# Kernel tuning notes

Hardware: AMD Instinct MI355X
Metric: run time of the kernel (lower is better)

Reference implementation:

```python
import jax, jax.numpy as jnp
import numpy as np

V, E, H, L, B, T = 50000, 512, 512, 32, 64, 512


def _lstm_dir(xg, w_hh, reverse):
    # xg: [B,T,4H] precomputed input-to-gate projections (+ biases)
    b, t, g4 = xg.shape
    h_dim = g4 // 4
    def step(carry, xt):
        h, c = carry
        g = xt + h @ w_hh.T  # [B,4H], PyTorch gate order i,f,g,o
        i, f, gg, o = jnp.split(g, 4, axis=-1)
        c = jax.nn.sigmoid(f) * c + jax.nn.sigmoid(i) * jnp.tanh(gg)
        h = jax.nn.sigmoid(o) * jnp.tanh(c)
        return (h, c), h
    init = (jnp.zeros((b, h_dim), xg.dtype), jnp.zeros((b, h_dim), xg.dtype))
    _, hs = jax.lax.scan(step, init, jnp.swapaxes(xg, 0, 1), reverse=reverse)
    return jnp.swapaxes(hs, 0, 1)  # [B,T,H]


def _bilstm(x, w_ih0, w_ih1, w_hh, b_ih, b_hh):
    w_ihs = (w_ih0, w_ih1)
    for l in range(2):
        outs = []
        for d in range(2):  # 0=forward, 1=backward
            xg = jnp.einsum('bti,gi->btg', x, w_ihs[l][d]) + b_ih[l, d] + b_hh[l, d]
            outs.append(_lstm_dir(xg, w_hh[l, d], reverse=(d == 1)))
        x = jnp.concatenate(outs, axis=-1)  # [B,T,2H]
    return x


def _crf_nll(emissions, tags, start, end, trans):
    # pytorch-crf: returns sum log-likelihood; module returns its negation.
    emit = jnp.take_along_axis(emissions, tags[..., None], axis=-1)[..., 0]  # [B,T]
    num = (start[tags[:, 0]] + emit.sum(1)
           + trans[tags[:, :-1], tags[:, 1:]].sum(1) + end[tags[:, -1]])
    alpha0 = start + emissions[:, 0]  # [B,L]
    def step(alpha, e_t):
        s = alpha[:, :, None] + trans[None] + e_t[:, None, :]  # [B,L,L]
        return jax.nn.logsumexp(s, axis=1), None
    alpha, _ = jax.lax.scan(step, alpha0, jnp.swapaxes(emissions[:, 1:], 0, 1))
    denom = jax.nn.logsumexp(alpha + end, axis=-1)  # [B]
    return -(num - denom).sum()


def setup_inputs() -> dict:
    key = jax.random.key(0)
    ks = jax.random.split(key, 13)
    s = 0.05
    emb = jax.random.normal(ks[0], (V, E), jnp.float32) * s
    emb = emb.at[0].set(0.0)  # padding_idx=0
    return {
        'datas': jax.random.randint(ks[1], (B, T), 0, V, jnp.int32),
        'labels': jax.random.randint(ks[2], (B, T), 0, L, jnp.int32),
        'emb': emb,
        'w_ih0': jax.random.normal(ks[3], (2, 4 * H, E), jnp.float32) * s,
        'w_ih1': jax.random.normal(ks[4], (2, 4 * H, 2 * H), jnp.float32) * s,
        'w_hh': jax.random.normal(ks[5], (2, 2, 4 * H, H), jnp.float32) * s,
        'b_ih': jax.random.normal(ks[6], (2, 2, 4 * H), jnp.float32) * s,
        'b_hh': jax.random.normal(ks[7], (2, 2, 4 * H), jnp.float32) * s,
        'w_out': jax.random.normal(ks[8], (2 * H, L), jnp.float32) * s,
        'b_out': jax.random.normal(ks[9], (L,), jnp.float32) * s,
        'crf_start': jax.random.normal(ks[10], (L,), jnp.float32) * s,
        'crf_end': jax.random.normal(ks[11], (L,), jnp.float32) * s,
        'crf_trans': jax.random.normal(ks[12], (L, L), jnp.float32) * s,
    }


def reference(datas, labels, emb, w_ih0, w_ih1, w_hh, b_ih, b_hh, w_out, b_out,
              crf_start, crf_end, crf_trans):
    x = emb[datas]  # [B,T,E]
    h = _bilstm(x, w_ih0, w_ih1, w_hh, b_ih, b_hh)  # [B,T,2H]; dropout=0 (eval)
    emissions = h @ w_out + b_out  # [B,T,L]
    return _crf_nll(emissions, labels, crf_start, crf_end, crf_trans)
```

## Files before the change

kernel.cpp:

```cpp
#include <hip/hip_runtime.h>

typedef unsigned short ushort_t;
typedef unsigned long long u64_t;
typedef __attribute__((ext_vector_type(8))) short short8;
typedef __attribute__((ext_vector_type(4))) float floatx4;


__device__ __forceinline__ float bf2f(ushort_t u) {
  unsigned x = ((unsigned)u) << 16;
  return __builtin_bit_cast(float, x);
}
__device__ __forceinline__ ushort_t f2bf(float f) {
  unsigned x = __builtin_bit_cast(unsigned, f);
  x += 0x7FFFu + ((x >> 16) & 1u);
  return (ushort_t)(x >> 16);
}
__device__ __forceinline__ float sigf(float x) { return 1.0f / (1.0f + __expf(-x)); }
__device__ __forceinline__ float tanhf_(float x) { return 1.0f - 2.0f / (__expf(2.0f * x) + 1.0f); }

static const size_t OFF_A    = 0;
static const size_t OFF_OUT0 = 67108864;
static const size_t OFF_XG   = 134217728;
static const size_t OFF_WIH0 = 167772160;
static const size_t OFF_WIH1 = 171966464;
static const size_t OFF_BIAS = 180355072;
static const size_t OFF_WOUT = 180387840;
static const size_t OFF_HC   = 180453376;
static const size_t OFF_CST  = 181501952;
static const size_t OFF_BAR  = 182026240;
static const size_t OFF_NUM  = 182059008;
static const size_t OFF_PERB = 182059264;
static const size_t OFF_END  = 182059520;

__global__ void prep_kernel(const float* __restrict__ w_ih0, const float* __restrict__ w_ih1,
                            const float* __restrict__ b_ih, const float* __restrict__ b_hh,
                            const float* __restrict__ w_out,
                            ushort_t* __restrict__ wih0_bf, ushort_t* __restrict__ wih1_bf,
                            float* __restrict__ bias, ushort_t* __restrict__ wout_bf) {
  int idx = blockIdx.x * 256 + threadIdx.x;
  int stride = gridDim.x * 256;
  for (int i = idx; i < 2097152; i += stride) wih0_bf[i] = f2bf(w_ih0[i]);
  for (int i = idx; i < 4194304; i += stride) wih1_bf[i] = f2bf(w_ih1[i]);
  for (int i = idx; i < 8192; i += stride) bias[i] = b_ih[i] + b_hh[i];
  for (int i = idx; i < 32768; i += stride) {
    int j = i & 7, Ls = (i >> 3) & 63, kb = (i >> 9) & 31, nt = i >> 14;
    int n = nt * 16 + (Ls & 15);
    int k = kb * 32 + ((Ls >> 4) & 3) * 8 + j;
    wout_bf[i] = f2bf(w_out[k * 32 + n]);
  }
}

__global__ void embed_kernel(const int* __restrict__ datas, const float* __restrict__ emb,
                             ushort_t* __restrict__ x_bf) {
  int idx = blockIdx.x * 256 + threadIdx.x;
  int row = idx >> 6, sub = idx & 63;
  int tok = datas[row];
  const float4* ep = (const float4*)(emb + (size_t)tok * 512 + sub * 8);
  float4 f0 = ep[0], f1 = ep[1];
  short8 v;
  v[0] = (short)f2bf(f0.x); v[1] = (short)f2bf(f0.y);
  v[2] = (short)f2bf(f0.z); v[3] = (short)f2bf(f0.w);
  v[4] = (short)f2bf(f1.x); v[5] = (short)f2bf(f1.y);
  v[6] = (short)f2bf(f1.z); v[7] = (short)f2bf(f1.w);
  *(short8*)(x_bf + (size_t)row * 512 + sub * 8) = v;
}

__device__ __forceinline__ void gemm_body(ushort_t* alds, ushort_t* blds, int gid, int tid,
                                          const ushort_t* __restrict__ A, int K,
                                          const ushort_t* __restrict__ W,
                                          const float* __restrict__ biasL,
                                          ushort_t* __restrict__ xg0,
                                          ushort_t* __restrict__ xg1,
                                          int t00, int t01) {
  int dir = gid >> 9, r = gid & 511;
  int mt = r & 31, ntt = r >> 5;
  int t0 = dir ? t01 : t00;
  const ushort_t* Bm = W + (size_t)dir * 2048 * K;
  const float* bptr = biasL + dir * 2048;
  ushort_t* xg = dir ? xg1 : xg0;
  int bm0 = mt * 128, bn0 = ntt * 128;
  int L = tid & 63, w = tid >> 6;
  int wm = w & 1, wn = w >> 1;
  floatx4 acc[4][4] = {};
  for (int k0 = 0; k0 < K; k0 += 32) {
    __syncthreads();
    #pragma unroll
    for (int rep = 0; rep < 2; rep++) {
      int slot = rep * 256 + tid;
      int t8 = slot >> 6, Ls = slot & 63;
      int col = k0 + (Ls >> 4) * 8;
      int mp = bm0 + t8 * 16 + (Ls & 15);
      int Arow = (mp >> 6) * 512 + t0 + (mp & 63);
      *(short8*)&alds[slot * 8] = *(const short8*)&A[(size_t)Arow * K + col];
      int rowb = bn0 + t8 * 16 + (Ls & 15);
      *(short8*)&blds[slot * 8] = *(const short8*)&Bm[(size_t)rowb * K + col];
    }
    __syncthreads();
    short8 af[4];
    #pragma unroll
    for (int a = 0; a < 4; a++) af[a] = *(const short8*)&alds[((wm * 4 + a) * 64 + L) * 8];
    #pragma unroll
    for (int bq = 0; bq < 4; bq++) {
      short8 bfr = *(const short8*)&blds[((wn * 4 + bq) * 64 + L) * 8];
      #pragma unroll
      for (int a = 0; a < 4; a++)
        acc[a][bq] = __builtin_amdgcn_mfma_f32_16x16x32_bf16(af[a], bfr, acc[a][bq], 0, 0, 0);
    }
  }
  int lm = L >> 4, ln = L & 15;
  #pragma unroll
  for (int bq = 0; bq < 4; bq++) {
    int n = bn0 + (wn * 4 + bq) * 16 + ln;
    float bv = bptr[n];
    #pragma unroll
    for (int a = 0; a < 4; a++) {
      #pragma unroll
      for (int rr = 0; rr < 4; rr++) {
        int m = bm0 + (wm * 4 + a) * 16 + lm * 4 + rr;
        int b = m >> 6, ts = m & 63;
        xg[((size_t)(ts * 64 + b)) * 2048 + n] = f2bf(acc[a][bq][rr] + bv);
      }
    }
  }
}

__global__ __launch_bounds__(256) void gemm_chunk(const ushort_t* __restrict__ A, int K,
                                                  const ushort_t* __restrict__ W,
                                                  const float* __restrict__ biasL,
                                                  ushort_t* __restrict__ xg0c,
                                                  ushort_t* __restrict__ xg1c,
                                                  int t00, int t01) {
  __shared__ alignas(16) ushort_t alds[512 * 8];
  __shared__ alignas(16) ushort_t blds[512 * 8];
  gemm_body(alds, blds, blockIdx.x, threadIdx.x, A, K, W, biasL, xg0c, xg1c, t00, t01);
}

__device__ __forceinline__ void lstm_body(ushort_t* wlds, int bid, int tid,
                                          const ushort_t* __restrict__ xg0c,
                                          const ushort_t* __restrict__ xg1c,
                                          const float* __restrict__ whh_f,
                                          ushort_t* __restrict__ hcL,
                                          float* __restrict__ cstL,
                                          ushort_t* __restrict__ outL,
                                          int* __restrict__ barF, int c) {
  int d = bid >> 5, g = bid & 31, j0 = g * 16;
  int L = tid & 63, w = tid >> 6;
  const float* wptr = whh_f + (size_t)d * 2048 * 512;
  #pragma unroll
  for (int it = 0; it < 16; it++) {
    int slot = it * 256 + tid;
    int q = slot >> 10, kb = (slot >> 6) & 15, Ls = slot & 63;
    int gcol = q * 512 + j0 + (Ls & 15);
    int k = kb * 32 + (Ls >> 4) * 8;
    const float* src = wptr + (size_t)gcol * 512 + k;
    float4 f0 = *(const float4*)src;
    float4 f1 = *(const float4*)(src + 4);
    short8 v;
    v[0] = (short)f2bf(f0.x); v[1] = (short)f2bf(f0.y);
    v[2] = (short)f2bf(f0.z); v[3] = (short)f2bf(f0.w);
    v[4] = (short)f2bf(f1.x); v[5] = (short)f2bf(f1.y);
    v[6] = (short)f2bf(f1.z); v[7] = (short)f2bf(f1.w);
    *(short8*)&wlds[slot * 8] = v;
  }
  __syncthreads();
  const ushort_t* xgd = d ? xg1c : xg0c;
  ushort_t* hcd = hcL + (size_t)d * 2 * 32768;
  int* flg = barF + d * 2048;
  int* myflag = flg + (g * 4 + w) * 16;
  const int* pollp = flg + ((L & 31) * 4 + w) * 16;
  bool pact = (L < 32);
  int q8 = L >> 4, jj = L & 15;
  int mbase = w * 16 + q8 * 4;
  int wslot = ((w * 16 + (g >> 1)) * 64 + q8 * 4 + 16 * ((g & 1) * 2 + (jj >> 3))) * 8 + (jj & 7);
  int rbase = (w * 16 * 64 + L) * 8;
  float cv[4];
  #pragma unroll
  for (int rr = 0; rr < 4; rr++) cv[rr] = cstL[(size_t)d * 32768 + (mbase + rr) * 512 + j0 + jj];

  auto ldxg = [&](int sl2, ushort_t dst[4][4]) {
    int ts2 = d ? (63 - sl2) : sl2;
    #pragma unroll
    for (int rr = 0; rr < 4; rr++) {
      const ushort_t* xrow = xgd + ((size_t)(ts2 * 64 + mbase + rr)) * 2048 + j0 + jj;
      #pragma unroll
      for (int q = 0; q < 4; q++) dst[q][rr] = xrow[q * 512];
    }
  };

  ushort_t xgu[4][4];
  ldxg(0, xgu);

  for (int sl = 0; sl < 64; sl++) {
    int s = c * 64 + sl;
    int t = d ? (511 - s) : s;
    const u64_t* h64 = (const u64_t*)(hcd + (size_t)(s & 1) * 32768);
    unsigned* h32w = (unsigned*)(hcd + (size_t)((s + 1) & 1) * 32768);
    int b64 = rbase >> 2;
    u64_t hv[32];
    #pragma unroll
    for (int kb = 0; kb < 16; kb++) {
      hv[2 * kb]     = __hip_atomic_load(h64 + b64 + kb * 128,     __ATOMIC_RELAXED, __HIP_MEMORY_SCOPE_AGENT);
      hv[2 * kb + 1] = __hip_atomic_load(h64 + b64 + kb * 128 + 1, __ATOMIC_RELAXED, __HIP_MEMORY_SCOPE_AGENT);
    }
    floatx4 acc[4] = {};
    #pragma unroll
    for (int kb = 0; kb < 16; kb++) {
      union { u64_t u[2]; short8 v; } pk;
      pk.u[0] = hv[2 * kb];
      pk.u[1] = hv[2 * kb + 1];
      short8 a = pk.v;
      #pragma unroll
      for (int q = 0; q < 4; q++) {
        short8 bfr = *(const short8*)&wlds[((q * 16 + kb) * 64 + L) * 8];
        acc[q] = __builtin_amdgcn_mfma_f32_16x16x32_bf16(a, bfr, acc[q], 0, 0, 0);
      }
    }
    ushort_t hbv[4];
    #pragma unroll
    for (int rr = 0; rr < 4; rr++) {
      float ii = acc[0][rr] + bf2f(xgu[0][rr]);
      float ff = acc[1][rr] + bf2f(xgu[1][rr]);
      float gg = acc[2][rr] + bf2f(xgu[2][rr]);
      float oo = acc[3][rr] + bf2f(xgu[3][rr]);
      float cc = sigf(ff) * cv[rr] + sigf(ii) * tanhf_(gg);
      cv[rr] = cc;
      hbv[rr] = f2bf(sigf(oo) * tanhf_(cc));
    }
    bool evn = (jj & 1) == 0;
    unsigned pk4[4];
    #pragma unroll
    for (int rr = 0; rr < 4; rr++) {
      unsigned mine = (unsigned)hbv[rr];
      unsigned nb = (unsigned)__shfl_xor((int)mine, 1, 64);
      pk4[rr] = mine | (nb << 16);
      if (evn)
        __hip_atomic_store(h32w + ((wslot + rr * 8) >> 1), pk4[rr],
                           __ATOMIC_RELAXED, __HIP_MEMORY_SCOPE_AGENT);
    }
    if (sl != 63) {
      asm volatile("s_waitcnt vmcnt(0)" ::: "memory");
      if (L == 0)
        __hip_atomic_store(myflag, s + 1, __ATOMIC_RELAXED, __HIP_MEMORY_SCOPE_AGENT);
      if (evn) {
        #pragma unroll
        for (int rr = 0; rr < 4; rr++) {
          int m = mbase + rr;
          *(unsigned*)&outL[((size_t)m * 512 + t) * 1024 + (d << 9) + j0 + jj] = pk4[rr];
        }
      }
      ldxg(sl + 1, xgu);
      int target = s + 1, guard = 0;
      while (guard < (1 << 17)) {
        int f = pact ? __hip_atomic_load(pollp, __ATOMIC_RELAXED, __HIP_MEMORY_SCOPE_AGENT)
                     : target;
        if (__ballot(f >= target) == ~0ULL) break;
        guard++;
      }
    } else {
      if (evn) {
        #pragma unroll
        for (int rr = 0; rr < 4; rr++) {
          int m = mbase + rr;
          *(unsigned*)&outL[((size_t)m * 512 + t) * 1024 + (d << 9) + j0 + jj] = pk4[rr];
        }
      }
    }
  }
  #pragma unroll
  for (int rr = 0; rr < 4; rr++) cstL[(size_t)d * 32768 + (mbase + rr) * 512 + j0 + jj] = cv[rr];
}

__global__ __launch_bounds__(256) void lstm_chunk(const ushort_t* __restrict__ xg0c,
                                                  const ushort_t* __restrict__ xg1c,
                                                  const float* __restrict__ whh_f,
                                                  ushort_t* __restrict__ hcL,
                                                  float* __restrict__ cstL,
                                                  ushort_t* __restrict__ outL,
                                                  int* __restrict__ barF, int c) {
  __shared__ alignas(16) ushort_t wlds[32768];
  lstm_body(wlds, blockIdx.x, threadIdx.x, xg0c, xg1c, whh_f, hcL, cstL, outL, barF, c);
}

__global__ __launch_bounds__(256) void fused_chunk(
    const ushort_t* __restrict__ l_xg0, const ushort_t* __restrict__ l_xg1,
    const float* __restrict__ whh_f, ushort_t* __restrict__ hcL,
    float* __restrict__ cstL, ushort_t* __restrict__ outL,
    int* __restrict__ barF, int c,
    const ushort_t* __restrict__ g_A, int g_K,
    const ushort_t* __restrict__ g_W, const float* __restrict__ g_bias,
    ushort_t* __restrict__ g_xg0, ushort_t* __restrict__ g_xg1,
    int g_t00, int g_t01) {
  __shared__ alignas(16) ushort_t lds[32768];
  if (blockIdx.x < 64) {
    lstm_body(lds, blockIdx.x, threadIdx.x, l_xg0, l_xg1, whh_f, hcL, cstL, outL, barF, c);
  } else {
    gemm_body(lds, lds + 4096, blockIdx.x - 64, threadIdx.x,
              g_A, g_K, g_W, g_bias, g_xg0, g_xg1, g_t00, g_t01);
  }
}

__global__ __launch_bounds__(256) void emis_kernel(const ushort_t* __restrict__ out1,
                                                   const ushort_t* __restrict__ wout_bf,
                                                   const float* __restrict__ b_out,
                                                   float* __restrict__ emis) {
  int tid = threadIdx.x, L = tid & 63, w = tid >> 6;
  int bm0 = blockIdx.x * 128;
  int q8 = L >> 4, ln = L & 15;
  floatx4 acc[2][2] = {};
  #pragma unroll 4
  for (int kb = 0; kb < 32; kb++) {
    short8 a0 = *(const short8*)&out1[(size_t)(bm0 + (w * 2 + 0) * 16 + ln) * 1024 + kb * 32 + q8 * 8];
    short8 a1 = *(const short8*)&out1[(size_t)(bm0 + (w * 2 + 1) * 16 + ln) * 1024 + kb * 32 + q8 * 8];
    #pragma unroll
    for (int nt = 0; nt < 2; nt++) {
      short8 bfr = *(const short8*)&wout_bf[((size_t)(nt * 32 + kb) * 64 + L) * 8];
      acc[0][nt] = __builtin_amdgcn_mfma_f32_16x16x32_bf16(a0, bfr, acc[0][nt], 0, 0, 0);
      acc[1][nt] = __builtin_amdgcn_mfma_f32_16x16x32_bf16(a1, bfr, acc[1][nt], 0, 0, 0);
    }
  }
  #pragma unroll
  for (int mt = 0; mt < 2; mt++) {
    #pragma unroll
    for (int nt = 0; nt < 2; nt++) {
      int n = nt * 16 + ln;
      float bv = b_out[n];
      #pragma unroll
      for (int rr = 0; rr < 4; rr++) {
        int m = bm0 + (w * 2 + mt) * 16 + q8 * 4 + rr;
        emis[(size_t)m * 32 + n] = acc[mt][nt][rr] + bv;
      }
    }
  }
}

__global__ void num_kernel(const int* __restrict__ labels, const float* __restrict__ emis,
                           const float* __restrict__ trans, const float* __restrict__ cstart,
                           const float* __restrict__ cend, float* __restrict__ num) {
  int b = blockIdx.x, tid = threadIdx.x;
  float s = 0.f;
  for (int t = tid; t < 512; t += 64) {
    int tag = labels[b * 512 + t];
    s += emis[(size_t)(b * 512 + t) * 32 + tag];
    if (t < 511) s += trans[tag * 32 + labels[b * 512 + t + 1]];
  }
  #pragma unroll
  for (int off = 32; off > 0; off >>= 1) s += __shfl_xor(s, off, 64);
  if (tid == 0) num[b] = s + cstart[labels[b * 512]] + cend[labels[b * 512 + 511]];
}

__global__ __launch_bounds__(64) void fwd_kernel(const float* __restrict__ emis,
                                                 const float* __restrict__ trans,
                                                 const float* __restrict__ cstart,
                                                 const float* __restrict__ cend,
                                                 const float* __restrict__ num,
                                                 float* __restrict__ perb) {
  int b = blockIdx.x, tid = threadIdx.x, j = tid & 31;
  float etr[32];
  #pragma unroll
  for (int i = 0; i < 32; i++) etr[i] = __expf(trans[i * 32 + j]);
  float alpha = cstart[j] + emis[(size_t)(b * 512) * 32 + j];
  float e_cur = emis[(size_t)(b * 512 + 1) * 32 + j];
  for (int t = 1; t < 512; t++) {
    float e_nx = (t < 511) ? emis[(size_t)(b * 512 + t + 1) * 32 + j] : 0.f;
    float mA = alpha;
    mA = fmaxf(mA, __shfl_xor(mA, 1, 32));
    mA = fmaxf(mA, __shfl_xor(mA, 2, 32));
    mA = fmaxf(mA, __shfl_xor(mA, 4, 32));
    mA = fmaxf(mA, __shfl_xor(mA, 8, 32));
    mA = fmaxf(mA, __shfl_xor(mA, 16, 32));
    float p = __expf(alpha - mA);
    float s0 = 0.f, s1 = 0.f, s2 = 0.f, s3 = 0.f;
    #pragma unroll
    for (int i = 0; i < 32; i += 4) {
      s0 = fmaf(__shfl(p, i, 32),     etr[i],     s0);
      s1 = fmaf(__shfl(p, i + 1, 32), etr[i + 1], s1);
      s2 = fmaf(__shfl(p, i + 2, 32), etr[i + 2], s2);
      s3 = fmaf(__shfl(p, i + 3, 32), etr[i + 3], s3);
    }
    alpha = __logf((s0 + s1) + (s2 + s3)) + mA + e_cur;
    e_cur = e_nx;
  }
  float z = alpha + cend[j];
  float m2 = z;
  #pragma unroll
  for (int off = 16; off > 0; off >>= 1) m2 = fmaxf(m2, __shfl_xor(m2, off, 32));
  float s2r = __expf(z - m2);
  #pragma unroll
  for (int off = 16; off > 0; off >>= 1) s2r += __shfl_xor(s2r, off, 32);
  if (tid == 0) perb[b] = num[b] - (__logf(s2r) + m2);
}

__global__ void final_kernel(const float* __restrict__ perb, float* __restrict__ out) {
  int tid = threadIdx.x;
  float s = perb[tid];
  #pragma unroll
  for (int off = 32; off > 0; off >>= 1) s += __shfl_xor(s, off, 64);
  if (tid == 0) out[0] = -s;
}

extern "C" void kernel_launch(void* const* d_in, const int* in_sizes, int n_in,
                              void* d_out, int out_size, void* d_ws, size_t ws_size,
                              hipStream_t stream) {
  (void)in_sizes; (void)n_in; (void)out_size;
  const int* datas = (const int*)d_in[0];
  const int* labels = (const int*)d_in[1];
  const float* emb = (const float*)d_in[2];
  const float* w_ih0 = (const float*)d_in[3];
  const float* w_ih1 = (const float*)d_in[4];
  const float* w_hh = (const float*)d_in[5];
  const float* b_ih = (const float*)d_in[6];
  const float* b_hh = (const float*)d_in[7];
  const float* w_out = (const float*)d_in[8];
  const float* b_out = (const float*)d_in[9];
  const float* cstart = (const float*)d_in[10];
  const float* cend = (const float*)d_in[11];
  const float* ctrans = (const float*)d_in[12];

  char* ws = (char*)d_ws;
  ushort_t* x_bf = (ushort_t*)(ws + OFF_A);
  ushort_t* out1 = (ushort_t*)(ws + OFF_A);
  ushort_t* out0 = (ushort_t*)(ws + OFF_OUT0);
  ushort_t* xA0 = (ushort_t*)(ws + OFF_XG);
  ushort_t* xA1 = (ushort_t*)(ws + OFF_XG + 16777216);
  ushort_t* xB0a = (ushort_t*)(ws + OFF_A + 33554432);
  ushort_t* xB0b = (ushort_t*)(ws + OFF_A + 50331648);
  ushort_t* xB1a = (ushort_t*)(ws + OFF_END);
  ushort_t* xB1b = (ushort_t*)(ws + OFF_END + 16777216);
  bool big = ws_size >= OFF_END + 33554432ull;
  float* emis = (float*)(ws + OFF_XG);
  ushort_t* wih0_bf = (ushort_t*)(ws + OFF_WIH0);
  ushort_t* wih1_bf = (ushort_t*)(ws + OFF_WIH1);
  float* bias = (float*)(ws + OFF_BIAS);
  ushort_t* wout_bf = (ushort_t*)(ws + OFF_WOUT);
  ushort_t* hc0 = (ushort_t*)(ws + OFF_HC);
  ushort_t* hc1 = hc0 + 131072;
  float* cst0 = (float*)(ws + OFF_CST);
  float* cst1 = cst0 + 65536;
  int* bar = (int*)(ws + OFF_BAR);
  float* numb = (float*)(ws + OFF_NUM);
  float* perb = (float*)(ws + OFF_PERB);

  hipMemsetAsync(ws + OFF_HC, 0, OFF_END - OFF_HC, stream);

  prep_kernel<<<2048, 256, 0, stream>>>(w_ih0, w_ih1, b_ih, b_hh, w_out,
                                        wih0_bf, wih1_bf, bias, wout_bf);
  embed_kernel<<<8192, 256, 0, stream>>>(datas, emb, x_bf);

  gemm_chunk<<<1024, 256, 0, stream>>>(x_bf, 512, wih0_bf, bias, xA0, xA1, 0, 448);
  for (int c = 0; c < 8; c++) {
    ushort_t* r0 = (c & 1) ? xB0a : xA0;
    ushort_t* r1 = (c & 1) ? xB0b : xA1;
    if (c < 7) {
      ushort_t* w0 = ((c + 1) & 1) ? xB0a : xA0;
      ushort_t* w1 = ((c + 1) & 1) ? xB0b : xA1;
      fused_chunk<<<1088, 256, 0, stream>>>(r0, r1, w_hh, hc0, cst0, out0, bar, c,
                                            x_bf, 512, wih0_bf, bias, w0, w1,
                                            (c + 1) * 64, (6 - c) * 64);
    } else {
      lstm_chunk<<<64, 256, 0, stream>>>(r0, r1, w_hh, hc0, cst0, out0, bar, c);
    }
  }

  gemm_chunk<<<1024, 256, 0, stream>>>(out0, 1024, wih1_bf, bias + 4096, xA0, xA1, 0, 448);
  for (int c = 0; c < 8; c++) {
    if (big) {
      ushort_t* r0 = (c & 1) ? xB1a : xA0;
      ushort_t* r1 = (c & 1) ? xB1b : xA1;
      if (c < 7) {
        ushort_t* w0 = ((c + 1) & 1) ? xB1a : xA0;
        ushort_t* w1 = ((c + 1) & 1) ? xB1b : xA1;
        fused_chunk<<<1088, 256, 0, stream>>>(r0, r1, w_hh + 2097152, hc1, cst1, out1,
                                              bar + 4096, c,
                                              out0, 1024, wih1_bf, bias + 4096, w0, w1,
                                              (c + 1) * 64, (6 - c) * 64);
      } else {
        lstm_chunk<<<64, 256, 0, stream>>>(r0, r1, w_hh + 2097152, hc1, cst1, out1,
                                           bar + 4096, c);
      }
    } else {
      lstm_chunk<<<64, 256, 0, stream>>>(xA0, xA1, w_hh + 2097152, hc1, cst1, out1,
                                         bar + 4096, c);
      if (c < 7)
        gemm_chunk<<<1024, 256, 0, stream>>>(out0, 1024, wih1_bf, bias + 4096, xA0, xA1,
                                             (c + 1) * 64, (6 - c) * 64);
    }
  }

  emis_kernel<<<256, 256, 0, stream>>>(out1, wout_bf, b_out, emis);
  num_kernel<<<64, 64, 0, stream>>>(labels, emis, ctrans, cstart, cend, numb);
  fwd_kernel<<<64, 64, 0, stream>>>(emis, ctrans, cstart, cend, numb, perb);
  final_kernel<<<1, 64, 0, stream>>>(perb, (float*)d_out);
}
```

Before: 4.919 ms.

## Fuse prep/embed and num/fwd kernels, interleave gate layout, pipeline barrier polling

Merges the weight-prep and embedding-gather kernels into one launch, and folds the CRF numerator computation into the forward-algorithm kernel, removing two launches. Changes the xg gate-projection layout so the four gates for a hidden unit are adjacent, letting the LSTM step load them with a single 8-byte vector load instead of four strided scalar loads. Also restructures the spin-wait so the next flag load is issued before the previous value is checked, hiding some of the poll latency. The barrier change may add one extra iteration of polling latency per exit.

```diff
diff --git a/kernel.cpp b/kernel.cpp
--- a/kernel.cpp
+++ b/kernel.cpp
@@ -3,6 +3,7 @@
 typedef unsigned short ushort_t;
 typedef unsigned long long u64_t;
 typedef __attribute__((ext_vector_type(8))) short short8;
+typedef __attribute__((ext_vector_type(4))) short short4v;
 typedef __attribute__((ext_vector_type(4))) float floatx4;
 
 
@@ -32,13 +33,27 @@
 static const size_t OFF_PERB = 182059264;
 static const size_t OFF_END  = 182059520;
 
-__global__ void prep_kernel(const float* __restrict__ w_ih0, const float* __restrict__ w_ih1,
-                            const float* __restrict__ b_ih, const float* __restrict__ b_hh,
-                            const float* __restrict__ w_out,
-                            ushort_t* __restrict__ wih0_bf, ushort_t* __restrict__ wih1_bf,
-                            float* __restrict__ bias, ushort_t* __restrict__ wout_bf) {
+__global__ void prep_embed(const int* __restrict__ datas, const float* __restrict__ emb,
+                           ushort_t* __restrict__ x_bf,
+                           const float* __restrict__ w_ih0, const float* __restrict__ w_ih1,
+                           const float* __restrict__ b_ih, const float* __restrict__ b_hh,
+                           const float* __restrict__ w_out,
+                           ushort_t* __restrict__ wih0_bf, ushort_t* __restrict__ wih1_bf,
+                           float* __restrict__ bias, ushort_t* __restrict__ wout_bf) {
   int idx = blockIdx.x * 256 + threadIdx.x;
   int stride = gridDim.x * 256;
+  for (int i = idx; i < 2097152; i += stride) {
+    int row = i >> 6, sub = i & 63;
+    int tok = datas[row];
+    const float4* ep = (const float4*)(emb + (size_t)tok * 512 + sub * 8);
+    float4 f0 = ep[0], f1 = ep[1];
+    short8 v;
+    v[0] = (short)f2bf(f0.x); v[1] = (short)f2bf(f0.y);
+    v[2] = (short)f2bf(f0.z); v[3] = (short)f2bf(f0.w);
+    v[4] = (short)f2bf(f1.x); v[5] = (short)f2bf(f1.y);
+    v[6] = (short)f2bf(f1.z); v[7] = (short)f2bf(f1.w);
+    *(short8*)(x_bf + (size_t)row * 512 + sub * 8) = v;
+  }
   for (int i = idx; i < 2097152; i += stride) wih0_bf[i] = f2bf(w_ih0[i]);
   for (int i = idx; i < 4194304; i += stride) wih1_bf[i] = f2bf(w_ih1[i]);
   for (int i = idx; i < 8192; i += stride) bias[i] = b_ih[i] + b_hh[i];
@@ -48,21 +63,6 @@
     int k = kb * 32 + ((Ls >> 4) & 3) * 8 + j;
     wout_bf[i] = f2bf(w_out[k * 32 + n]);
   }
-}
-
-__global__ void embed_kernel(const int* __restrict__ datas, const float* __restrict__ emb,
-                             ushort_t* __restrict__ x_bf) {
-  int idx = blockIdx.x * 256 + threadIdx.x;
-  int row = idx >> 6, sub = idx & 63;
-  int tok = datas[row];
-  const float4* ep = (const float4*)(emb + (size_t)tok * 512 + sub * 8);
-  float4 f0 = ep[0], f1 = ep[1];
-  short8 v;
-  v[0] = (short)f2bf(f0.x); v[1] = (short)f2bf(f0.y);
-  v[2] = (short)f2bf(f0.z); v[3] = (short)f2bf(f0.w);
-  v[4] = (short)f2bf(f1.x); v[5] = (short)f2bf(f1.y);
-  v[6] = (short)f2bf(f1.z); v[7] = (short)f2bf(f1.w);
-  *(short8*)(x_bf + (size_t)row * 512 + sub * 8) = v;
 }
 
 __device__ __forceinline__ void gemm_body(ushort_t* alds, ushort_t* blds, int gid, int tid,
@@ -112,13 +112,14 @@
   for (int bq = 0; bq < 4; bq++) {
     int n = bn0 + (wn * 4 + bq) * 16 + ln;
     float bv = bptr[n];
+    int nidx = ((n & 511) << 2) + (n >> 9);
     #pragma unroll
     for (int a = 0; a < 4; a++) {
       #pragma unroll
       for (int rr = 0; rr < 4; rr++) {
         int m = bm0 + (wm * 4 + a) * 16 + lm * 4 + rr;
         int b = m >> 6, ts = m & 63;
-        xg[((size_t)(ts * 64 + b)) * 2048 + n] = f2bf(acc[a][bq][rr] + bv);
+        xg[((size_t)(ts * 64 + b)) * 2048 + nidx] = f2bf(acc[a][bq][rr] + bv);
       }
     }
   }
@@ -181,9 +182,11 @@
     int ts2 = d ? (63 - sl2) : sl2;
     #pragma unroll
     for (int rr = 0; rr < 4; rr++) {
-      const ushort_t* xrow = xgd + ((size_t)(ts2 * 64 + mbase + rr)) * 2048 + j0 + jj;
+      const short4v* xrow = (const short4v*)(xgd + ((size_t)(ts2 * 64 + mbase + rr)) * 2048
+                                             + ((j0 + jj) << 2));
+      short4v v = *xrow;
       #pragma unroll
-      for (int q = 0; q < 4; q++) dst[q][rr] = xrow[q * 512];
+      for (int q = 0; q < 4; q++) dst[q][rr] = (ushort_t)v[q];
     }
   };
 
@@ -250,10 +253,13 @@
       }
       ldxg(sl + 1, xgu);
       int target = s + 1, guard = 0;
+      int f0 = pact ? __hip_atomic_load(pollp, __ATOMIC_RELAXED, __HIP_MEMORY_SCOPE_AGENT)
+                    : target;
       while (guard < (1 << 17)) {
-        int f = pact ? __hip_atomic_load(pollp, __ATOMIC_RELAXED, __HIP_MEMORY_SCOPE_AGENT)
-                     : target;
-        if (__ballot(f >= target) == ~0ULL) break;
+        int f1 = pact ? __hip_atomic_load(pollp, __ATOMIC_RELAXED, __HIP_MEMORY_SCOPE_AGENT)
+                      : target;
+        if (__ballot(f0 >= target) == ~0ULL) break;
+        f0 = f1;
         guard++;
       }
     } else {
@@ -333,28 +339,22 @@
   }
 }
 
-__global__ void num_kernel(const int* __restrict__ labels, const float* __restrict__ emis,
-                           const float* __restrict__ trans, const float* __restrict__ cstart,
-                           const float* __restrict__ cend, float* __restrict__ num) {
-  int b = blockIdx.x, tid = threadIdx.x;
-  float s = 0.f;
-  for (int t = tid; t < 512; t += 64) {
-    int tag = labels[b * 512 + t];
-    s += emis[(size_t)(b * 512 + t) * 32 + tag];
-    if (t < 511) s += trans[tag * 32 + labels[b * 512 + t + 1]];
-  }
-  #pragma unroll
-  for (int off = 32; off > 0; off >>= 1) s += __shfl_xor(s, off, 64);
-  if (tid == 0) num[b] = s + cstart[labels[b * 512]] + cend[labels[b * 512 + 511]];
-}
-
-__global__ __launch_bounds__(64) void fwd_kernel(const float* __restrict__ emis,
+__global__ __launch_bounds__(64) void fwd_kernel(const int* __restrict__ labels,
+                                                 const float* __restrict__ emis,
                                                  const float* __restrict__ trans,
                                                  const float* __restrict__ cstart,
                                                  const float* __restrict__ cend,
-                                                 const float* __restrict__ num,
                                                  float* __restrict__ perb) {
   int b = blockIdx.x, tid = threadIdx.x, j = tid & 31;
+  float sn = 0.f;
+  for (int t = tid; t < 512; t += 64) {
+    int tag = labels[b * 512 + t];
+    sn += emis[(size_t)(b * 512 + t) * 32 + tag];
+    if (t < 511) sn += trans[tag * 32 + labels[b * 512 + t + 1]];
+  }
+  #pragma unroll
+  for (int off = 32; off > 0; off >>= 1) sn += __shfl_xor(sn, off, 64);
+  sn += cstart[labels[b * 512]] + cend[labels[b * 512 + 511]];
   float etr[32];
   #pragma unroll
   for (int i = 0; i < 32; i++) etr[i] = __expf(trans[i * 32 + j]);
@@ -387,7 +387,7 @@
   float s2r = __expf(z - m2);
   #pragma unroll
   for (int off = 16; off > 0; off >>= 1) s2r += __shfl_xor(s2r, off, 32);
-  if (tid == 0) perb[b] = num[b] - (__logf(s2r) + m2);
+  if (tid == 0) perb[b] = sn - (__logf(s2r) + m2);
 }
 
 __global__ void final_kernel(const float* __restrict__ perb, float* __restrict__ out) {
@@ -437,14 +437,12 @@
   float* cst0 = (float*)(ws + OFF_CST);
   float* cst1 = cst0 + 65536;
   int* bar = (int*)(ws + OFF_BAR);
-  float* numb = (float*)(ws + OFF_NUM);
   float* perb = (float*)(ws + OFF_PERB);
 
   hipMemsetAsync(ws + OFF_HC, 0, OFF_END - OFF_HC, stream);
 
-  prep_kernel<<<2048, 256, 0, stream>>>(w_ih0, w_ih1, b_ih, b_hh, w_out,
-                                        wih0_bf, wih1_bf, bias, wout_bf);
-  embed_kernel<<<8192, 256, 0, stream>>>(datas, emb, x_bf);
+  prep_embed<<<8192, 256, 0, stream>>>(datas, emb, x_bf, w_ih0, w_ih1, b_ih, b_hh, w_out,
+                                       wih0_bf, wih1_bf, bias, wout_bf);
 
   gemm_chunk<<<1024, 256, 0, stream>>>(x_bf, 512, wih0_bf, bias, xA0, xA1, 0, 448);
   for (int c = 0; c < 8; c++) {
@@ -487,7 +485,6 @@
   }
 
   emis_kernel<<<256, 256, 0, stream>>>(out1, wout_bf, b_out, emis);
-  num_kernel<<<64, 64, 0, stream>>>(labels, emis, ctrans, cstart, cend, numb);
-  fwd_kernel<<<64, 64, 0, stream>>>(emis, ctrans, cstart, cend, numb, perb);
+  fwd_kernel<<<64, 64, 0, stream>>>(labels, emis, ctrans, cstart, cend, perb);
   final_kernel<<<1, 64, 0, stream>>>(perb, (float*)d_out);
 }
```

New measurement: 5.582 ms. 1.13x slower.
